# Kernel tuning notes

Measured on AMD Instinct MI355X. Metric: run time of the kernel, lower is better.

The kernel has to match this reference:

```python
import jax, jax.numpy as jnp
import numpy as np

# --- Clifford algebra constants for a 4D Euclidean space (MULTIVECTOR_DIM = 16) ---
# grades 0..4 have dims (1,4,6,4,1); component index -> grade:
GRADE_OF = np.array([0] + [1]*4 + [2]*6 + [3]*4 + [4], dtype=np.int64)  # [16]
# reversion sign per grade k: (-1)^{k(k-1)/2}
_REV_PER_GRADE = np.array([1.0, 1.0, -1.0, -1.0, 1.0], dtype=np.float32)
REVERSION = jnp.asarray(_REV_PER_GRADE[GRADE_OF])            # [16]
# scalar part of geometric product of orthonormal basis blades: diag of reversion signs
SCALAR_TABLE = jnp.asarray(np.diag(_REV_PER_GRADE[GRADE_OF]).astype(np.float32))  # [16,16]
SCALE = 1.0 / np.sqrt(16.0)

B, S, H, M = 4, 2048, 8, 16


def _block_masks():
    block = (GRADE_OF[:, None] == GRADE_OF[None, :]).astype(np.float32)  # [16,16]
    bias = ((GRADE_OF == 0) | (GRADE_OF == 4)).astype(np.float32)        # [16]
    return jnp.asarray(block), jnp.asarray(bias)


def setup_inputs() -> dict:
    key = jax.random.key(0)
    ks = jax.random.split(key, 10)
    block, bias = _block_masks()
    def w_in(k):   # [16, H, 16], zero outside grade blocks (j -> i within same grade)
        return jax.random.normal(k, (M, H, M), jnp.float32) * 0.1 * block[:, None, :]
    def b_in(k):   # [H, 16], only grade-0 / grade-4 components have bias
        return jax.random.normal(k, (H, M), jnp.float32) * 0.1 * bias[None, :]
    x = jax.random.normal(ks[0], (B, S, M), jnp.float32)
    return {
        "x": x,
        "wq": w_in(ks[1]), "bq": b_in(ks[2]),
        "wk": w_in(ks[3]), "bk": b_in(ks[4]),
        "wv": w_in(ks[5]), "bv": b_in(ks[6]),
        "wo": jax.random.normal(ks[7], (H, M, M), jnp.float32) * 0.1 * block[None, :, :],
        "bo": jax.random.normal(ks[8], (M,), jnp.float32) * 0.1 * bias,
    }


def reference(x, wq, bq, wk, bk, wv, bv, wo, bo):
    # per-grade Q/K/V projections, packed as block-sparse linears over 16 components
    q = jnp.einsum('bsj,jhi->bhsi', x, wq) + bq[None, :, None, :]  # [B,H,S,16]
    k = jnp.einsum('bsj,jhi->bhsi', x, wk) + bk[None, :, None, :]
    v = jnp.einsum('bsj,jhi->bhsi', x, wv) + bv[None, :, None, :]
    k_rev = k * REVERSION[None, None, None, :]
    # scalar part of geometric product <Q * reverse(K)>_0 via fixed bilinear table
    scores = jnp.einsum('bhqi,bhkj,ij->bhqk', q, k_rev, SCALAR_TABLE) * SCALE
    attn = jax.nn.softmax(scores, axis=-1)                         # [B,H,S,S]
    head = jnp.einsum('bhqk,bhki->bhqi', attn, v)                  # [B,H,S,16]
    # per-grade output projections (block over heads x grade components)
    out = jnp.einsum('bhqj,hji->bqi', head, wo) + bo               # [B,S,16]
    return out
```

## Files before the change

kernel.cpp:

```cpp
#include <hip/hip_runtime.h>

#define BB 4
#define SS 2048
#define HH 8
#define MM 16

#define QSCALE 0.36067376022224085f

typedef __attribute__((ext_vector_type(8)))  short short8;
typedef __attribute__((ext_vector_type(4)))  int   int4v;
typedef __attribute__((ext_vector_type(4)))  float f32x4;
typedef __attribute__((ext_vector_type(16))) float f32x16;

static constexpr size_t NQKV = (size_t)BB * HH * SS * MM;

__device__ __forceinline__ int pk_bf16(float lo, float hi) {
    int r;
    asm("v_cvt_pk_bf16_f32 %0, %1, %2" : "=v"(r) : "v"(lo), "v"(hi));
    return r;
}

__device__ __forceinline__ void proj16(const float xr[16], const float* __restrict__ w,
                                       const float* __restrict__ bias, int h, float out[16]) {
#pragma unroll
    for (int i = 0; i < 16; i++) out[i] = bias[(h << 4) + i];
#pragma unroll
    for (int j = 0; j < 16; j++) {
        float xj = xr[j];
        const float* wr = w + (((j * HH) + h) << 4);
#pragma unroll
        for (int i = 0; i < 16; i++) out[i] = fmaf(xj, wr[i], out[i]);
    }
}

__device__ __forceinline__ void pack_store(ushort* dst, const float o[16], float scale) {
    int4v w0, w1;
#pragma unroll
    for (int j = 0; j < 4; j++) w0[j] = pk_bf16(o[2*j] * scale,     o[2*j+1] * scale);
#pragma unroll
    for (int j = 0; j < 4; j++) w1[j] = pk_bf16(o[8+2*j] * scale,   o[8+2*j+1] * scale);
    int4v* p = (int4v*)dst;
    p[0] = w0; p[1] = w1;
}

__global__ __launch_bounds__(256) void proj_kernel(
    const float* __restrict__ x,
    const float* __restrict__ wq, const float* __restrict__ bq,
    const float* __restrict__ wk, const float* __restrict__ bk,
    const float* __restrict__ wv, const float* __restrict__ bv,
    ushort* __restrict__ qb, ushort* __restrict__ kb, ushort* __restrict__ vb)
{
    int h  = blockIdx.x >> 5;
    int bs = ((blockIdx.x & 31) << 8) + threadIdx.x;
    int b  = bs >> 11;

    float xr[16];
    const float4* x4 = (const float4*)(x + (size_t)bs * MM);
#pragma unroll
    for (int j = 0; j < 4; j++) {
        float4 t = x4[j];
        xr[j*4+0] = t.x; xr[j*4+1] = t.y; xr[j*4+2] = t.z; xr[j*4+3] = t.w;
    }

    size_t orow = (((size_t)(b * HH + h) * SS) + (bs & 2047)) * MM;
    float o[16];

    proj16(xr, wq, bq, h, o);  pack_store(qb + orow, o, QSCALE);
    proj16(xr, wk, bk, h, o);  pack_store(kb + orow, o, 1.0f);
    proj16(xr, wv, bv, h, o);  pack_store(vb + orow, o, 1.0f);
}

__global__ __launch_bounds__(512) void attn_kernel(
    const ushort* __restrict__ qb, const ushort* __restrict__ kb,
    const ushort* __restrict__ vb, float* __restrict__ hb)
{
    __shared__ ushort stage[4][3840];

    int tid = threadIdx.x;
    int grp = tid >> 7, t7 = tid & 127;
    int wid2 = (tid >> 6) & 1;
    int lane = tid & 63;
    int n = lane & 31, c = lane >> 5;

    int nb = ((blockIdx.x & 7) << 7) | (blockIdx.x >> 3);
    int bh = nb >> 5, qt = nb & 31;
    size_t base = (size_t)bh * SS * MM;
    const ushort* Qg = qb + base;
    const ushort* Kg = kb + base;
    const ushort* Vg = vb + base;

    int q = qt * 64 + wid2 * 32 + n;
    short8 qf = *(const short8*)(Qg + (size_t)q * MM + c * 8);

    ushort* Kl = &stage[grp][0];
    ushort* Vt = &stage[grp][1536];

    for (int i = t7; i < 72; i += 128) {
        Vt[16 * 72 + i] = 0x3F80;
        Vt[20 * 72 + i] = 0x3F80;
#pragma unroll
        for (int r = 17; r < 20; r++) Vt[r * 72 + i] = 0;
#pragma unroll
        for (int r = 21; r < 32; r++) Vt[r * 72 + i] = 0;
    }

    int k0 = grp * 512;
    int srow = t7 >> 1, shalf = t7 & 1;

    {
        int4v kw = *(const int4v*)(Kg + (size_t)(k0 + srow) * MM + shalf * 8);
        int4v vw = *(const int4v*)(Vg + (size_t)(k0 + srow) * MM + shalf * 8);
        *(int4v*)&Kl[srow * 24 + shalf * 8] = kw;
        union { int4v v; ushort s[8]; } vu; vu.v = vw;
#pragma unroll
        for (int j = 0; j < 8; j++) Vt[(8 * shalf + j) * 72 + srow] = vu.s[j];
    }
    __syncthreads();

    f32x16 oacc = 0;
    const f32x16 zacc = 0;
    float cs = 0.0f;
    int csd = lane >> 2, cspart = lane & 3;

    for (int t = 0; t < 8; t++) {
        int4v kw2, vw2;
        if (t != 7) {
            kw2 = *(const int4v*)(Kg + (size_t)(k0 + (t + 1) * 64 + srow) * MM + shalf * 8);
            vw2 = *(const int4v*)(Vg + (size_t)(k0 + (t + 1) * 64 + srow) * MM + shalf * 8);
        }

#pragma unroll
        for (int sub = 0; sub < 2; sub++) {
            short8 kf = *(const short8*)&Kl[(sub * 32 + n) * 24 + c * 8];
            short8 vf1 = *(const short8*)&Vt[n * 72 + sub * 32 + c * 8];
            short8 vf2 = *(const short8*)&Vt[n * 72 + sub * 32 + 16 + c * 8];
            f32x16 s = __builtin_amdgcn_mfma_f32_32x32x16_bf16(kf, qf, zacc, 0, 0, 0);

            float p0 = __builtin_amdgcn_exp2f(s[0])  - 1.0f;
            float p1 = __builtin_amdgcn_exp2f(s[1])  - 1.0f;
            float p2 = __builtin_amdgcn_exp2f(s[2])  - 1.0f;
            float p3 = __builtin_amdgcn_exp2f(s[3])  - 1.0f;
            float p4 = __builtin_amdgcn_exp2f(s[4])  - 1.0f;
            float p5 = __builtin_amdgcn_exp2f(s[5])  - 1.0f;
            float p6 = __builtin_amdgcn_exp2f(s[6])  - 1.0f;
            float p7 = __builtin_amdgcn_exp2f(s[7])  - 1.0f;
            int a0 = pk_bf16(p0, p1), a1 = pk_bf16(p2, p3);
            int a2 = pk_bf16(p4, p5), a3 = pk_bf16(p6, p7);
            int w0 = a0, w2 = a2;
            asm("v_permlane32_swap_b32 %0, %1" : "+v"(w0), "+v"(w2));
            int w1 = a1, w3 = a3;
            asm("v_permlane32_swap_b32 %0, %1" : "+v"(w1), "+v"(w3));
            int4v bi1 = {w0, w1, w2, w3};
            short8 B1 = __builtin_bit_cast(short8, bi1);
            oacc = __builtin_amdgcn_mfma_f32_32x32x16_bf16(vf1, B1, oacc, 0, 0, 0);

            float p8  = __builtin_amdgcn_exp2f(s[8])  - 1.0f;
            float p9  = __builtin_amdgcn_exp2f(s[9])  - 1.0f;
            float p10 = __builtin_amdgcn_exp2f(s[10]) - 1.0f;
            float p11 = __builtin_amdgcn_exp2f(s[11]) - 1.0f;
            float p12 = __builtin_amdgcn_exp2f(s[12]) - 1.0f;
            float p13 = __builtin_amdgcn_exp2f(s[13]) - 1.0f;
            float p14 = __builtin_amdgcn_exp2f(s[14]) - 1.0f;
            float p15 = __builtin_amdgcn_exp2f(s[15]) - 1.0f;
            int a4 = pk_bf16(p8,  p9),  a5 = pk_bf16(p10, p11);
            int a6 = pk_bf16(p12, p13), a7 = pk_bf16(p14, p15);
            int u0 = a4, u2 = a6;
            asm("v_permlane32_swap_b32 %0, %1" : "+v"(u0), "+v"(u2));
            int u1 = a5, u3 = a7;
            asm("v_permlane32_swap_b32 %0, %1" : "+v"(u1), "+v"(u3));
            int4v bi2 = {u0, u1, u2, u3};
            short8 B2 = __builtin_bit_cast(short8, bi2);
            oacc = __builtin_amdgcn_mfma_f32_32x32x16_bf16(vf2, B2, oacc, 0, 0, 0);
        }

        {
            int4v u0 = *(const int4v*)&Vt[csd * 72 + cspart * 16];
            int4v u1 = *(const int4v*)&Vt[csd * 72 + cspart * 16 + 8];
#pragma unroll
            for (int j = 0; j < 4; j++) {
                cs += __builtin_bit_cast(float, u0[j] << 16);
                cs += __builtin_bit_cast(float, (int)(u0[j] & 0xFFFF0000));
                cs += __builtin_bit_cast(float, u1[j] << 16);
                cs += __builtin_bit_cast(float, (int)(u1[j] & 0xFFFF0000));
            }
        }

        __syncthreads();
        if (t != 7) {
            *(int4v*)&Kl[srow * 24 + shalf * 8] = kw2;
            union { int4v v; ushort s[8]; } vu; vu.v = vw2;
#pragma unroll
            for (int j = 0; j < 8; j++) Vt[(8 * shalf + j) * 72 + srow] = vu.s[j];
        }
        __syncthreads();
    }

    cs += __shfl_xor(cs, 1);
    cs += __shfl_xor(cs, 2);

    float* mgf = (float*)&stage[0][0];
    int ql = wid2 * 32 + n;
    if (grp != 0) {
        float* dst = mgf + (size_t)(grp - 1) * 1152 + ql * 18;
#pragma unroll
        for (int j = 0; j < 4; j++) dst[4 * c + j]     = oacc[j];
#pragma unroll
        for (int j = 0; j < 4; j++) dst[8 + 4 * c + j] = oacc[4 + j];
        dst[16 + c] = oacc[8];
    }
    if (wid2 == 0 && cspart == 0) mgf[3456 + grp * 16 + csd] = cs;
    __syncthreads();

    if (grp == 0) {
        float l = oacc[8];
        float o0[4], o1[4];
#pragma unroll
        for (int j = 0; j < 4; j++) { o0[j] = oacc[j]; o1[j] = oacc[4 + j]; }
#pragma unroll
        for (int p = 0; p < 3; p++) {
            const float* src = mgf + (size_t)p * 1152 + ql * 18;
#pragma unroll
            for (int j = 0; j < 4; j++) o0[j] += src[4 * c + j];
#pragma unroll
            for (int j = 0; j < 4; j++) o1[j] += src[8 + 4 * c + j];
            l += src[16 + c];
        }
#pragma unroll
        for (int w = 0; w < 4; w++) {
#pragma unroll
            for (int j = 0; j < 4; j++) o0[j] += mgf[3456 + w * 16 + 4 * c + j];
#pragma unroll
            for (int j = 0; j < 4; j++) o1[j] += mgf[3456 + w * 16 + 8 + 4 * c + j];
        }
        l += 2048.0f;

        float inv = 1.0f / l;
        float* orow = hb + base + (size_t)q * MM;
        f32x4 v0 = {o0[0] * inv, o0[1] * inv, o0[2] * inv, o0[3] * inv};
        f32x4 v1 = {o1[0] * inv, o1[1] * inv, o1[2] * inv, o1[3] * inv};
        *(f32x4*)(orow + 4 * c) = v0;
        *(f32x4*)(orow + 8 + 4 * c) = v1;
    }
}

__global__ __launch_bounds__(128) void outproj_kernel(
    const float* __restrict__ hb, const float* __restrict__ wo,
    const float* __restrict__ bo, float* __restrict__ out)
{
    int tid = threadIdx.x;
    int row = blockIdx.x * 64 + (tid >> 1);
    int hh = tid & 1;
    int b = row >> 11, s = row & 2047;

    float acc[16];
#pragma unroll
    for (int i = 0; i < 16; i++) acc[i] = 0.0f;

    for (int hi = 0; hi < 4; hi++) {
        int h = hh * 4 + hi;
        const float* hr = hb + ((size_t)(b * 8 + h) * SS + s) * MM;
        float hv[16];
        const f32x4* h4 = (const f32x4*)hr;
#pragma unroll
        for (int j = 0; j < 4; j++) {
            f32x4 tv = h4[j];
            hv[j*4+0] = tv[0]; hv[j*4+1] = tv[1]; hv[j*4+2] = tv[2]; hv[j*4+3] = tv[3];
        }
#pragma unroll
        for (int j = 0; j < 16; j++) {
            float hj = hv[j];
            const float* wr = wo + (((h << 4) + j) << 4);
#pragma unroll
            for (int i = 0; i < 16; i++) acc[i] = fmaf(hj, wr[i], acc[i]);
        }
    }

#pragma unroll
    for (int i = 0; i < 16; i++) acc[i] += __shfl_xor(acc[i], 1);

    if (hh == 0) {
        float* op = out + (size_t)row * MM;
#pragma unroll
        for (int j = 0; j < 4; j++) {
            f32x4 v = {acc[4*j+0] + bo[4*j+0], acc[4*j+1] + bo[4*j+1],
                       acc[4*j+2] + bo[4*j+2], acc[4*j+3] + bo[4*j+3]};
            *(f32x4*)(op + 4*j) = v;
        }
    }
}

extern "C" void kernel_launch(void* const* d_in, const int* in_sizes, int n_in,
                              void* d_out, int out_size, void* d_ws, size_t ws_size,
                              hipStream_t stream) {
    const float* x  = (const float*)d_in[0];
    const float* wq = (const float*)d_in[1];
    const float* bq = (const float*)d_in[2];
    const float* wk = (const float*)d_in[3];
    const float* bk = (const float*)d_in[4];
    const float* wv = (const float*)d_in[5];
    const float* bv = (const float*)d_in[6];
    const float* wo = (const float*)d_in[7];
    const float* bo = (const float*)d_in[8];
    float* out = (float*)d_out;

    ushort* qb = (ushort*)d_ws;
    ushort* kb = qb + NQKV;
    ushort* vb = kb + NQKV;
    float*  hb = (float*)(vb + NQKV);

    proj_kernel<<<256, 256, 0, stream>>>(x, wq, bq, wk, bk, wv, bv, qb, kb, vb);
    attn_kernel<<<1024, 512, 0, stream>>>(qb, kb, vb, hb);
    outproj_kernel<<<128, 128, 0, stream>>>(hb, wo, bo, out);
}
```

Baseline: 52.70 us.

## Process two query tiles per wave with double-buffered 128-key K/V stages

Each wave now holds two 32-query fragments and reuses every K/V fragment loaded from LDS for both, halving LDS reads per score. Keys are split across 2 groups instead of 4, with 128-key tiles that are double-buffered, so one barrier per iteration replaces two. Blocks shrink to 256 threads and the grid to 512 blocks, which lowers the number of waves available to hide latency and raises register pressure from the two accumulators.

Result: no change. 52.53 us (-0.3%).

```diff
diff --git a/kernel.cpp b/kernel.cpp
--- a/kernel.cpp
+++ b/kernel.cpp
@@ -70,112 +70,172 @@
     proj16(xr, wv, bv, h, o);  pack_store(vb + orow, o, 1.0f);
 }
 
-__global__ __launch_bounds__(512) void attn_kernel(
+__global__ __launch_bounds__(256) void attn_kernel(
     const ushort* __restrict__ qb, const ushort* __restrict__ kb,
     const ushort* __restrict__ vb, float* __restrict__ hb)
 {
-    __shared__ ushort stage[4][3840];
+    __shared__ ushort stage[2][2][7424];
 
     int tid = threadIdx.x;
-    int grp = tid >> 7, t7 = tid & 127;
-    int wid2 = (tid >> 6) & 1;
+    int w = tid >> 6, grp = w >> 1, qw = w & 1;
     int lane = tid & 63;
     int n = lane & 31, c = lane >> 5;
-
-    int nb = ((blockIdx.x & 7) << 7) | (blockIdx.x >> 3);
-    int bh = nb >> 5, qt = nb & 31;
+    int t7 = tid & 127;
+
+    int nb = ((blockIdx.x & 7) << 6) | (blockIdx.x >> 3);
+    int bh = nb >> 4, qt = nb & 15;
     size_t base = (size_t)bh * SS * MM;
     const ushort* Qg = qb + base;
     const ushort* Kg = kb + base;
     const ushort* Vg = vb + base;
 
-    int q = qt * 64 + wid2 * 32 + n;
-    short8 qf = *(const short8*)(Qg + (size_t)q * MM + c * 8);
-
-    ushort* Kl = &stage[grp][0];
-    ushort* Vt = &stage[grp][1536];
-
-    for (int i = t7; i < 72; i += 128) {
-        Vt[16 * 72 + i] = 0x3F80;
-        Vt[20 * 72 + i] = 0x3F80;
-#pragma unroll
-        for (int r = 17; r < 20; r++) Vt[r * 72 + i] = 0;
-#pragma unroll
-        for (int r = 21; r < 32; r++) Vt[r * 72 + i] = 0;
-    }
-
-    int k0 = grp * 512;
-    int srow = t7 >> 1, shalf = t7 & 1;
+    int qA = qt * 128 + qw * 64 + n;
+    int qB = qA + 32;
+    short8 qfA = *(const short8*)(Qg + (size_t)qA * MM + c * 8);
+    short8 qfB = *(const short8*)(Qg + (size_t)qB * MM + c * 8);
+
+#pragma unroll
+    for (int buf = 0; buf < 2; buf++) {
+        ushort* Vt = &stage[grp][buf][3072];
+        for (int i = t7; i < 136; i += 128) {
+            Vt[16 * 136 + i] = 0x3F80;
+            Vt[20 * 136 + i] = 0x3F80;
+#pragma unroll
+            for (int r = 17; r < 20; r++) Vt[r * 136 + i] = 0;
+#pragma unroll
+            for (int r = 21; r < 32; r++) Vt[r * 136 + i] = 0;
+        }
+    }
+
+    int k0 = grp * 1024;
+    int srow = t7;
 
     {
-        int4v kw = *(const int4v*)(Kg + (size_t)(k0 + srow) * MM + shalf * 8);
-        int4v vw = *(const int4v*)(Vg + (size_t)(k0 + srow) * MM + shalf * 8);
-        *(int4v*)&Kl[srow * 24 + shalf * 8] = kw;
-        union { int4v v; ushort s[8]; } vu; vu.v = vw;
-#pragma unroll
-        for (int j = 0; j < 8; j++) Vt[(8 * shalf + j) * 72 + srow] = vu.s[j];
+        const ushort* kr = Kg + (size_t)(k0 + srow) * MM;
+        const ushort* vr = Vg + (size_t)(k0 + srow) * MM;
+        int4v kw0 = *(const int4v*)(kr);
+        int4v kw1 = *(const int4v*)(kr + 8);
+        int4v vw0 = *(const int4v*)(vr);
+        int4v vw1 = *(const int4v*)(vr + 8);
+        ushort* Kl = &stage[grp][0][0];
+        ushort* Vt = &stage[grp][0][3072];
+        *(int4v*)&Kl[srow * 24]     = kw0;
+        *(int4v*)&Kl[srow * 24 + 8] = kw1;
+        union { int4v v; ushort s[8]; } ua, ub; ua.v = vw0; ub.v = vw1;
+#pragma unroll
+        for (int j = 0; j < 8; j++) Vt[j * 136 + srow]       = ua.s[j];
+#pragma unroll
+        for (int j = 0; j < 8; j++) Vt[(8 + j) * 136 + srow] = ub.s[j];
     }
     __syncthreads();
 
-    f32x16 oacc = 0;
+    f32x16 oaccA = 0, oaccB = 0;
     const f32x16 zacc = 0;
     float cs = 0.0f;
-    int csd = lane >> 2, cspart = lane & 3;
+    int csd = lane >> 2, csp = lane & 3;
 
     for (int t = 0; t < 8; t++) {
-        int4v kw2, vw2;
+        int cur = t & 1;
+        const ushort* Kl = &stage[grp][cur][0];
+        const ushort* Vt = &stage[grp][cur][3072];
+
+        int4v kw0, kw1, vw0, vw1;
         if (t != 7) {
-            kw2 = *(const int4v*)(Kg + (size_t)(k0 + (t + 1) * 64 + srow) * MM + shalf * 8);
-            vw2 = *(const int4v*)(Vg + (size_t)(k0 + (t + 1) * 64 + srow) * MM + shalf * 8);
-        }
-
-#pragma unroll
-        for (int sub = 0; sub < 2; sub++) {
-            short8 kf = *(const short8*)&Kl[(sub * 32 + n) * 24 + c * 8];
-            short8 vf1 = *(const short8*)&Vt[n * 72 + sub * 32 + c * 8];
-            short8 vf2 = *(const short8*)&Vt[n * 72 + sub * 32 + 16 + c * 8];
-            f32x16 s = __builtin_amdgcn_mfma_f32_32x32x16_bf16(kf, qf, zacc, 0, 0, 0);
-
-            float p0 = __builtin_amdgcn_exp2f(s[0])  - 1.0f;
-            float p1 = __builtin_amdgcn_exp2f(s[1])  - 1.0f;
-            float p2 = __builtin_amdgcn_exp2f(s[2])  - 1.0f;
-            float p3 = __builtin_amdgcn_exp2f(s[3])  - 1.0f;
-            float p4 = __builtin_amdgcn_exp2f(s[4])  - 1.0f;
-            float p5 = __builtin_amdgcn_exp2f(s[5])  - 1.0f;
-            float p6 = __builtin_amdgcn_exp2f(s[6])  - 1.0f;
-            float p7 = __builtin_amdgcn_exp2f(s[7])  - 1.0f;
-            int a0 = pk_bf16(p0, p1), a1 = pk_bf16(p2, p3);
-            int a2 = pk_bf16(p4, p5), a3 = pk_bf16(p6, p7);
-            int w0 = a0, w2 = a2;
-            asm("v_permlane32_swap_b32 %0, %1" : "+v"(w0), "+v"(w2));
-            int w1 = a1, w3 = a3;
-            asm("v_permlane32_swap_b32 %0, %1" : "+v"(w1), "+v"(w3));
-            int4v bi1 = {w0, w1, w2, w3};
-            short8 B1 = __builtin_bit_cast(short8, bi1);
-            oacc = __builtin_amdgcn_mfma_f32_32x32x16_bf16(vf1, B1, oacc, 0, 0, 0);
-
-            float p8  = __builtin_amdgcn_exp2f(s[8])  - 1.0f;
-            float p9  = __builtin_amdgcn_exp2f(s[9])  - 1.0f;
-            float p10 = __builtin_amdgcn_exp2f(s[10]) - 1.0f;
-            float p11 = __builtin_amdgcn_exp2f(s[11]) - 1.0f;
-            float p12 = __builtin_amdgcn_exp2f(s[12]) - 1.0f;
-            float p13 = __builtin_amdgcn_exp2f(s[13]) - 1.0f;
-            float p14 = __builtin_amdgcn_exp2f(s[14]) - 1.0f;
-            float p15 = __builtin_amdgcn_exp2f(s[15]) - 1.0f;
-            int a4 = pk_bf16(p8,  p9),  a5 = pk_bf16(p10, p11);
-            int a6 = pk_bf16(p12, p13), a7 = pk_bf16(p14, p15);
-            int u0 = a4, u2 = a6;
-            asm("v_permlane32_swap_b32 %0, %1" : "+v"(u0), "+v"(u2));
-            int u1 = a5, u3 = a7;
-            asm("v_permlane32_swap_b32 %0, %1" : "+v"(u1), "+v"(u3));
-            int4v bi2 = {u0, u1, u2, u3};
-            short8 B2 = __builtin_bit_cast(short8, bi2);
-            oacc = __builtin_amdgcn_mfma_f32_32x32x16_bf16(vf2, B2, oacc, 0, 0, 0);
+            const ushort* kr = Kg + (size_t)(k0 + (t + 1) * 128 + srow) * MM;
+            const ushort* vr = Vg + (size_t)(k0 + (t + 1) * 128 + srow) * MM;
+            kw0 = *(const int4v*)(kr);
+            kw1 = *(const int4v*)(kr + 8);
+            vw0 = *(const int4v*)(vr);
+            vw1 = *(const int4v*)(vr + 8);
+        }
+
+#pragma unroll
+        for (int sub = 0; sub < 4; sub++) {
+            short8 kf  = *(const short8*)&Kl[(sub * 32 + n) * 24 + c * 8];
+            short8 vf1 = *(const short8*)&Vt[n * 136 + sub * 32 + c * 8];
+            short8 vf2 = *(const short8*)&Vt[n * 136 + sub * 32 + 16 + c * 8];
+
+            f32x16 sA = __builtin_amdgcn_mfma_f32_32x32x16_bf16(kf, qfA, zacc, 0, 0, 0);
+            f32x16 sB = __builtin_amdgcn_mfma_f32_32x32x16_bf16(kf, qfB, zacc, 0, 0, 0);
+
+            {
+                float p0 = __builtin_amdgcn_exp2f(sA[0])  - 1.0f;
+                float p1 = __builtin_amdgcn_exp2f(sA[1])  - 1.0f;
+                float p2 = __builtin_amdgcn_exp2f(sA[2])  - 1.0f;
+                float p3 = __builtin_amdgcn_exp2f(sA[3])  - 1.0f;
+                float p4 = __builtin_amdgcn_exp2f(sA[4])  - 1.0f;
+                float p5 = __builtin_amdgcn_exp2f(sA[5])  - 1.0f;
+                float p6 = __builtin_amdgcn_exp2f(sA[6])  - 1.0f;
+                float p7 = __builtin_amdgcn_exp2f(sA[7])  - 1.0f;
+                int a0 = pk_bf16(p0, p1), a1 = pk_bf16(p2, p3);
+                int a2 = pk_bf16(p4, p5), a3 = pk_bf16(p6, p7);
+                int w0 = a0, w2 = a2;
+                asm("v_permlane32_swap_b32 %0, %1" : "+v"(w0), "+v"(w2));
+                int w1 = a1, w3 = a3;
+                asm("v_permlane32_swap_b32 %0, %1" : "+v"(w1), "+v"(w3));
+                int4v bi1 = {w0, w1, w2, w3};
+                oaccA = __builtin_amdgcn_mfma_f32_32x32x16_bf16(
+                    vf1, __builtin_bit_cast(short8, bi1), oaccA, 0, 0, 0);
+                float p8  = __builtin_amdgcn_exp2f(sA[8])  - 1.0f;
+                float p9  = __builtin_amdgcn_exp2f(sA[9])  - 1.0f;
+                float p10 = __builtin_amdgcn_exp2f(sA[10]) - 1.0f;
+                float p11 = __builtin_amdgcn_exp2f(sA[11]) - 1.0f;
+                float p12 = __builtin_amdgcn_exp2f(sA[12]) - 1.0f;
+                float p13 = __builtin_amdgcn_exp2f(sA[13]) - 1.0f;
+                float p14 = __builtin_amdgcn_exp2f(sA[14]) - 1.0f;
+                float p15 = __builtin_amdgcn_exp2f(sA[15]) - 1.0f;
+                int a4 = pk_bf16(p8,  p9),  a5 = pk_bf16(p10, p11);
+                int a6 = pk_bf16(p12, p13), a7 = pk_bf16(p14, p15);
+                int u0 = a4, u2 = a6;
+                asm("v_permlane32_swap_b32 %0, %1" : "+v"(u0), "+v"(u2));
+                int u1 = a5, u3 = a7;
+                asm("v_permlane32_swap_b32 %0, %1" : "+v"(u1), "+v"(u3));
+                int4v bi2 = {u0, u1, u2, u3};
+                oaccA = __builtin_amdgcn_mfma_f32_32x32x16_bf16(
+                    vf2, __builtin_bit_cast(short8, bi2), oaccA, 0, 0, 0);
+            }
+            {
+                float p0 = __builtin_amdgcn_exp2f(sB[0])  - 1.0f;
+                float p1 = __builtin_amdgcn_exp2f(sB[1])  - 1.0f;
+                float p2 = __builtin_amdgcn_exp2f(sB[2])  - 1.0f;
+                float p3 = __builtin_amdgcn_exp2f(sB[3])  - 1.0f;
+                float p4 = __builtin_amdgcn_exp2f(sB[4])  - 1.0f;
+                float p5 = __builtin_amdgcn_exp2f(sB[5])  - 1.0f;
+                float p6 = __builtin_amdgcn_exp2f(sB[6])  - 1.0f;
+                float p7 = __builtin_amdgcn_exp2f(sB[7])  - 1.0f;
+                int a0 = pk_bf16(p0, p1), a1 = pk_bf16(p2, p3);
+                int a2 = pk_bf16(p4, p5), a3 = pk_bf16(p6, p7);
+                int w0 = a0, w2 = a2;
+                asm("v_permlane32_swap_b32 %0, %1" : "+v"(w0), "+v"(w2));
+                int w1 = a1, w3 = a3;
+                asm("v_permlane32_swap_b32 %0, %1" : "+v"(w1), "+v"(w3));
+                int4v bi1 = {w0, w1, w2, w3};
+                oaccB = __builtin_amdgcn_mfma_f32_32x32x16_bf16(
+                    vf1, __builtin_bit_cast(short8, bi1), oaccB, 0, 0, 0);
+                float p8  = __builtin_amdgcn_exp2f(sB[8])  - 1.0f;
+                float p9  = __builtin_amdgcn_exp2f(sB[9])  - 1.0f;
+                float p10 = __builtin_amdgcn_exp2f(sB[10]) - 1.0f;
+                float p11 = __builtin_amdgcn_exp2f(sB[11]) - 1.0f;
+                float p12 = __builtin_amdgcn_exp2f(sB[12]) - 1.0f;
+                float p13 = __builtin_amdgcn_exp2f(sB[13]) - 1.0f;
+                float p14 = __builtin_amdgcn_exp2f(sB[14]) - 1.0f;
+                float p15 = __builtin_amdgcn_exp2f(sB[15]) - 1.0f;
+                int a4 = pk_bf16(p8,  p9),  a5 = pk_bf16(p10, p11);
+                int a6 = pk_bf16(p12, p13), a7 = pk_bf16(p14, p15);
+                int u0 = a4, u2 = a6;
+                asm("v_permlane32_swap_b32 %0, %1" : "+v"(u0), "+v"(u2));
+                int u1 = a5, u3 = a7;
+                asm("v_permlane32_swap_b32 %0, %1" : "+v"(u1), "+v"(u3));
+                int4v bi2 = {u0, u1, u2, u3};
+                oaccB = __builtin_amdgcn_mfma_f32_32x32x16_bf16(
+                    vf2, __builtin_bit_cast(short8, bi2), oaccB, 0, 0, 0);
+            }
         }
 
         {
-            int4v u0 = *(const int4v*)&Vt[csd * 72 + cspart * 16];
-            int4v u1 = *(const int4v*)&Vt[csd * 72 + cspart * 16 + 8];
+            const ushort* vrow = &Vt[csd * 136 + qw * 64 + csp * 16];
+            int4v u0 = *(const int4v*)(vrow);
+            int4v u1 = *(const int4v*)(vrow + 8);
 #pragma unroll
             for (int j = 0; j < 4; j++) {
                 cs += __builtin_bit_cast(float, u0[j] << 16);
@@ -185,12 +245,16 @@
             }
         }
 
-        __syncthreads();
         if (t != 7) {
-            *(int4v*)&Kl[srow * 24 + shalf * 8] = kw2;
-            union { int4v v; ushort s[8]; } vu; vu.v = vw2;
-#pragma unroll
-            for (int j = 0; j < 8; j++) Vt[(8 * shalf + j) * 72 + srow] = vu.s[j];
+            ushort* Kl2 = &stage[grp][cur ^ 1][0];
+            ushort* Vt2 = &stage[grp][cur ^ 1][3072];
+            *(int4v*)&Kl2[srow * 24]     = kw0;
+            *(int4v*)&Kl2[srow * 24 + 8] = kw1;
+            union { int4v v; ushort s[8]; } ua, ub; ua.v = vw0; ub.v = vw1;
+#pragma unroll
+            for (int j = 0; j < 8; j++) Vt2[j * 136 + srow]       = ua.s[j];
+#pragma unroll
+            for (int j = 0; j < 8; j++) Vt2[(8 + j) * 136 + srow] = ub.s[j];
         }
         __syncthreads();
     }
@@ -198,48 +262,71 @@
     cs += __shfl_xor(cs, 1);
     cs += __shfl_xor(cs, 2);
 
-    float* mgf = (float*)&stage[0][0];
-    int ql = wid2 * 32 + n;
-    if (grp != 0) {
-        float* dst = mgf + (size_t)(grp - 1) * 1152 + ql * 18;
-#pragma unroll
-        for (int j = 0; j < 4; j++) dst[4 * c + j]     = oacc[j];
-#pragma unroll
-        for (int j = 0; j < 4; j++) dst[8 + 4 * c + j] = oacc[4 + j];
-        dst[16 + c] = oacc[8];
-    }
-    if (wid2 == 0 && cspart == 0) mgf[3456 + grp * 16 + csd] = cs;
+    float* mgf = (float*)&stage[0][0][0];
+    int qlA = qw * 64 + n, qlB = qlA + 32;
+
+    if (grp == 1) {
+        float* dstA = mgf + qlA * 18;
+#pragma unroll
+        for (int j = 0; j < 4; j++) dstA[4 * c + j]     = oaccA[j];
+#pragma unroll
+        for (int j = 0; j < 4; j++) dstA[8 + 4 * c + j] = oaccA[4 + j];
+        dstA[16 + c] = oaccA[8];
+        float* dstB = mgf + qlB * 18;
+#pragma unroll
+        for (int j = 0; j < 4; j++) dstB[4 * c + j]     = oaccB[j];
+#pragma unroll
+        for (int j = 0; j < 4; j++) dstB[8 + 4 * c + j] = oaccB[4 + j];
+        dstB[16 + c] = oaccB[8];
+    }
+    if (csp == 0) mgf[2304 + (grp * 2 + qw) * 16 + csd] = cs;
     __syncthreads();
 
     if (grp == 0) {
-        float l = oacc[8];
-        float o0[4], o1[4];
-#pragma unroll
-        for (int j = 0; j < 4; j++) { o0[j] = oacc[j]; o1[j] = oacc[4 + j]; }
-#pragma unroll
-        for (int p = 0; p < 3; p++) {
-            const float* src = mgf + (size_t)p * 1152 + ql * 18;
-#pragma unroll
-            for (int j = 0; j < 4; j++) o0[j] += src[4 * c + j];
-#pragma unroll
-            for (int j = 0; j < 4; j++) o1[j] += src[8 + 4 * c + j];
-            l += src[16 + c];
-        }
-#pragma unroll
-        for (int w = 0; w < 4; w++) {
-#pragma unroll
-            for (int j = 0; j < 4; j++) o0[j] += mgf[3456 + w * 16 + 4 * c + j];
-#pragma unroll
-            for (int j = 0; j < 4; j++) o1[j] += mgf[3456 + w * 16 + 8 + 4 * c + j];
-        }
-        l += 2048.0f;
-
-        float inv = 1.0f / l;
-        float* orow = hb + base + (size_t)q * MM;
-        f32x4 v0 = {o0[0] * inv, o0[1] * inv, o0[2] * inv, o0[3] * inv};
-        f32x4 v1 = {o1[0] * inv, o1[1] * inv, o1[2] * inv, o1[3] * inv};
-        *(f32x4*)(orow + 4 * c) = v0;
-        *(f32x4*)(orow + 8 + 4 * c) = v1;
+        {
+            const float* src = mgf + qlA * 18;
+            float l = oaccA[8] + src[16 + c] + 2048.0f;
+            float o0[4], o1[4];
+#pragma unroll
+            for (int j = 0; j < 4; j++) o0[j] = oaccA[j]     + src[4 * c + j];
+#pragma unroll
+            for (int j = 0; j < 4; j++) o1[j] = oaccA[4 + j] + src[8 + 4 * c + j];
+#pragma unroll
+            for (int s = 0; s < 4; s++) {
+#pragma unroll
+                for (int j = 0; j < 4; j++) o0[j] += mgf[2304 + s * 16 + 4 * c + j];
+#pragma unroll
+                for (int j = 0; j < 4; j++) o1[j] += mgf[2304 + s * 16 + 8 + 4 * c + j];
+            }
+            float inv = 1.0f / l;
+            float* orow = hb + base + (size_t)qA * MM;
+            f32x4 v0 = {o0[0] * inv, o0[1] * inv, o0[2] * inv, o0[3] * inv};
+            f32x4 v1 = {o1[0] * inv, o1[1] * inv, o1[2] * inv, o1[3] * inv};
+            *(f32x4*)(orow + 4 * c) = v0;
+            *(f32x4*)(orow + 8 + 4 * c) = v1;
+        }
+        {
+            const float* src = mgf + qlB * 18;
+            float l = oaccB[8] + src[16 + c] + 2048.0f;
+            float o0[4], o1[4];
+#pragma unroll
+            for (int j = 0; j < 4; j++) o0[j] = oaccB[j]     + src[4 * c + j];
+#pragma unroll
+            for (int j = 0; j < 4; j++) o1[j] = oaccB[4 + j] + src[8 + 4 * c + j];
+#pragma unroll
+            for (int s = 0; s < 4; s++) {
+#pragma unroll
+                for (int j = 0; j < 4; j++) o0[j] += mgf[2304 + s * 16 + 4 * c + j];
+#pragma unroll
+                for (int j = 0; j < 4; j++) o1[j] += mgf[2304 + s * 16 + 8 + 4 * c + j];
+            }
+            float inv = 1.0f / l;
+            float* orow = hb + base + (size_t)qB * MM;
+            f32x4 v0 = {o0[0] * inv, o0[1] * inv, o0[2] * inv, o0[3] * inv};
+            f32x4 v1 = {o1[0] * inv, o1[1] * inv, o1[2] * inv, o1[3] * inv};
+            *(f32x4*)(orow + 4 * c) = v0;
+            *(f32x4*)(orow + 8 + 4 * c) = v1;
+        }
     }
 }
 
@@ -309,6 +396,6 @@
     float*  hb = (float*)(vb + NQKV);
 
     proj_kernel<<<256, 256, 0, stream>>>(x, wq, bq, wk, bk, wv, bv, qb, kb, vb);
-    attn_kernel<<<1024, 512, 0, stream>>>(qb, kb, vb, hb);
+    attn_kernel<<<512, 256, 0, stream>>>(qb, kb, vb, hb);
     outproj_kernel<<<128, 128, 0, stream>>>(hb, wo, bo, out);
 }
```

## Double attention K/V tile size, split warps by query half, widen outproj grid

Applied to the files above, without the earlier changes.

The attention kernel now stages 128 keys per tile instead of 64, using a new K layout split into two 8-column halves and a wider transposed V stride. This halves the loop trip count and removes one barrier per iteration. Each query-half warp now computes its own column sums, and a waves-per-EU hint of 6 is added to launch bounds. The output projection splits heads across 4 threads per row with an extra shuffle reduction and twice as many blocks, which raises parallelism. The cost is larger LDS use per block, which could limit occupancy.

Result: slower. 93.69 us (+77.8%).

```diff
diff --git a/kernel.cpp b/kernel.cpp
--- a/kernel.cpp
+++ b/kernel.cpp
@@ -70,17 +70,17 @@
     proj16(xr, wv, bv, h, o);  pack_store(vb + orow, o, 1.0f);
 }
 
-__global__ __launch_bounds__(512) void attn_kernel(
+__global__ __launch_bounds__(512, 6) void attn_kernel(
     const ushort* __restrict__ qb, const ushort* __restrict__ kb,
     const ushort* __restrict__ vb, float* __restrict__ hb)
 {
-    __shared__ ushort stage[4][3840];
+    __shared__ ushort stage[4][6400];
 
     int tid = threadIdx.x;
-    int grp = tid >> 7, t7 = tid & 127;
-    int wid2 = (tid >> 6) & 1;
+    int w = tid >> 6, grp = w >> 1, qw = w & 1;
     int lane = tid & 63;
     int n = lane & 31, c = lane >> 5;
+    int t7 = tid & 127;
 
     int nb = ((blockIdx.x & 7) << 7) | (blockIdx.x >> 3);
     int bh = nb >> 5, qt = nb & 31;
@@ -89,51 +89,63 @@
     const ushort* Kg = kb + base;
     const ushort* Vg = vb + base;
 
-    int q = qt * 64 + wid2 * 32 + n;
+    int q = qt * 64 + qw * 32 + n;
     short8 qf = *(const short8*)(Qg + (size_t)q * MM + c * 8);
 
     ushort* Kl = &stage[grp][0];
-    ushort* Vt = &stage[grp][1536];
-
-    for (int i = t7; i < 72; i += 128) {
-        Vt[16 * 72 + i] = 0x3F80;
-        Vt[20 * 72 + i] = 0x3F80;
-#pragma unroll
-        for (int r = 17; r < 20; r++) Vt[r * 72 + i] = 0;
-#pragma unroll
-        for (int r = 21; r < 32; r++) Vt[r * 72 + i] = 0;
+    ushort* Vt = &stage[grp][2048];
+
+    for (int i = t7; i < 136; i += 128) {
+        Vt[16 * 136 + i] = 0x3F80;
+        Vt[20 * 136 + i] = 0x3F80;
+#pragma unroll
+        for (int r = 17; r < 20; r++) Vt[r * 136 + i] = 0;
+#pragma unroll
+        for (int r = 21; r < 32; r++) Vt[r * 136 + i] = 0;
     }
 
     int k0 = grp * 512;
-    int srow = t7 >> 1, shalf = t7 & 1;
+    int srow = t7;
 
     {
-        int4v kw = *(const int4v*)(Kg + (size_t)(k0 + srow) * MM + shalf * 8);
-        int4v vw = *(const int4v*)(Vg + (size_t)(k0 + srow) * MM + shalf * 8);
-        *(int4v*)&Kl[srow * 24 + shalf * 8] = kw;
-        union { int4v v; ushort s[8]; } vu; vu.v = vw;
-#pragma unroll
-        for (int j = 0; j < 8; j++) Vt[(8 * shalf + j) * 72 + srow] = vu.s[j];
+        const ushort* kr = Kg + (size_t)(k0 + srow) * MM;
+        const ushort* vr = Vg + (size_t)(k0 + srow) * MM;
+        int4v kw0 = *(const int4v*)(kr);
+        int4v kw1 = *(const int4v*)(kr + 8);
+        int4v vw0 = *(const int4v*)(vr);
+        int4v vw1 = *(const int4v*)(vr + 8);
+        *(int4v*)&Kl[srow * 8]        = kw0;
+        *(int4v*)&Kl[1024 + srow * 8] = kw1;
+        union { int4v v; ushort s[8]; } ua, ub; ua.v = vw0; ub.v = vw1;
+#pragma unroll
+        for (int j = 0; j < 8; j++) Vt[j * 136 + srow]       = ua.s[j];
+#pragma unroll
+        for (int j = 0; j < 8; j++) Vt[(8 + j) * 136 + srow] = ub.s[j];
     }
     __syncthreads();
 
     f32x16 oacc = 0;
     const f32x16 zacc = 0;
     float cs = 0.0f;
-    int csd = lane >> 2, cspart = lane & 3;
-
-    for (int t = 0; t < 8; t++) {
-        int4v kw2, vw2;
-        if (t != 7) {
-            kw2 = *(const int4v*)(Kg + (size_t)(k0 + (t + 1) * 64 + srow) * MM + shalf * 8);
-            vw2 = *(const int4v*)(Vg + (size_t)(k0 + (t + 1) * 64 + srow) * MM + shalf * 8);
-        }
-
-#pragma unroll
-        for (int sub = 0; sub < 2; sub++) {
-            short8 kf = *(const short8*)&Kl[(sub * 32 + n) * 24 + c * 8];
-            short8 vf1 = *(const short8*)&Vt[n * 72 + sub * 32 + c * 8];
-            short8 vf2 = *(const short8*)&Vt[n * 72 + sub * 32 + 16 + c * 8];
+    int csd = lane >> 2, csp = lane & 3;
+
+    for (int t = 0; t < 4; t++) {
+        int4v kw0, kw1, vw0, vw1;
+        if (t != 3) {
+            const ushort* kr = Kg + (size_t)(k0 + (t + 1) * 128 + srow) * MM;
+            const ushort* vr = Vg + (size_t)(k0 + (t + 1) * 128 + srow) * MM;
+            kw0 = *(const int4v*)(kr);
+            kw1 = *(const int4v*)(kr + 8);
+            vw0 = *(const int4v*)(vr);
+            vw1 = *(const int4v*)(vr + 8);
+        }
+
+#pragma unroll
+        for (int sub = 0; sub < 4; sub++) {
+            short8 kf  = *(const short8*)&Kl[c * 1024 + (sub * 32 + n) * 8];
+            short8 vf1 = *(const short8*)&Vt[n * 136 + sub * 32 + c * 8];
+            short8 vf2 = *(const short8*)&Vt[n * 136 + sub * 32 + 16 + c * 8];
+
             f32x16 s = __builtin_amdgcn_mfma_f32_32x32x16_bf16(kf, qf, zacc, 0, 0, 0);
 
             float p0 = __builtin_amdgcn_exp2f(s[0])  - 1.0f;
@@ -151,8 +163,8 @@
             int w1 = a1, w3 = a3;
             asm("v_permlane32_swap_b32 %0, %1" : "+v"(w1), "+v"(w3));
             int4v bi1 = {w0, w1, w2, w3};
-            short8 B1 = __builtin_bit_cast(short8, bi1);
-            oacc = __builtin_amdgcn_mfma_f32_32x32x16_bf16(vf1, B1, oacc, 0, 0, 0);
+            oacc = __builtin_amdgcn_mfma_f32_32x32x16_bf16(
+                vf1, __builtin_bit_cast(short8, bi1), oacc, 0, 0, 0);
 
             float p8  = __builtin_amdgcn_exp2f(s[8])  - 1.0f;
             float p9  = __builtin_amdgcn_exp2f(s[9])  - 1.0f;
@@ -169,13 +181,14 @@
             int u1 = a5, u3 = a7;
             asm("v_permlane32_swap_b32 %0, %1" : "+v"(u1), "+v"(u3));
             int4v bi2 = {u0, u1, u2, u3};
-            short8 B2 = __builtin_bit_cast(short8, bi2);
-            oacc = __builtin_amdgcn_mfma_f32_32x32x16_bf16(vf2, B2, oacc, 0, 0, 0);
+            oacc = __builtin_amdgcn_mfma_f32_32x32x16_bf16(
+                vf2, __builtin_bit_cast(short8, bi2), oacc, 0, 0, 0);
         }
 
         {
-            int4v u0 = *(const int4v*)&Vt[csd * 72 + cspart * 16];
-            int4v u1 = *(const int4v*)&Vt[csd * 72 + cspart * 16 + 8];
+            const ushort* vrow = &Vt[csd * 136 + qw * 64 + csp * 16];
+            int4v u0 = *(const int4v*)(vrow);
+            int4v u1 = *(const int4v*)(vrow + 8);
 #pragma unroll
             for (int j = 0; j < 4; j++) {
                 cs += __builtin_bit_cast(float, u0[j] << 16);
@@ -186,20 +199,24 @@
         }
 
         __syncthreads();
-        if (t != 7) {
-            *(int4v*)&Kl[srow * 24 + shalf * 8] = kw2;
-            union { int4v v; ushort s[8]; } vu; vu.v = vw2;
-#pragma unroll
-            for (int j = 0; j < 8; j++) Vt[(8 * shalf + j) * 72 + srow] = vu.s[j];
-        }
-        __syncthreads();
+        if (t != 3) {
+            *(int4v*)&Kl[srow * 8]        = kw0;
+            *(int4v*)&Kl[1024 + srow * 8] = kw1;
+            union { int4v v; ushort s[8]; } ua, ub; ua.v = vw0; ub.v = vw1;
+#pragma unroll
+            for (int j = 0; j < 8; j++) Vt[j * 136 + srow]       = ua.s[j];
+#pragma unroll
+            for (int j = 0; j < 8; j++) Vt[(8 + j) * 136 + srow] = ub.s[j];
+            __syncthreads();
+        }
     }
 
     cs += __shfl_xor(cs, 1);
     cs += __shfl_xor(cs, 2);
 
     float* mgf = (float*)&stage[0][0];
-    int ql = wid2 * 32 + n;
+    int ql = qw * 32 + n;
+
     if (grp != 0) {
         float* dst = mgf + (size_t)(grp - 1) * 1152 + ql * 18;
 #pragma unroll
@@ -208,7 +225,7 @@
         for (int j = 0; j < 4; j++) dst[8 + 4 * c + j] = oacc[4 + j];
         dst[16 + c] = oacc[8];
     }
-    if (wid2 == 0 && cspart == 0) mgf[3456 + grp * 16 + csd] = cs;
+    if (csp == 0) mgf[3456 + (grp * 2 + qw) * 16 + csd] = cs;
     __syncthreads();
 
     if (grp == 0) {
@@ -226,11 +243,11 @@
             l += src[16 + c];
         }
 #pragma unroll
-        for (int w = 0; w < 4; w++) {
-#pragma unroll
-            for (int j = 0; j < 4; j++) o0[j] += mgf[3456 + w * 16 + 4 * c + j];
-#pragma unroll
-            for (int j = 0; j < 4; j++) o1[j] += mgf[3456 + w * 16 + 8 + 4 * c + j];
+        for (int s = 0; s < 8; s++) {
+#pragma unroll
+            for (int j = 0; j < 4; j++) o0[j] += mgf[3456 + s * 16 + 4 * c + j];
+#pragma unroll
+            for (int j = 0; j < 4; j++) o1[j] += mgf[3456 + s * 16 + 8 + 4 * c + j];
         }
         l += 2048.0f;
 
@@ -248,16 +265,17 @@
     const float* __restrict__ bo, float* __restrict__ out)
 {
     int tid = threadIdx.x;
-    int row = blockIdx.x * 64 + (tid >> 1);
-    int hh = tid & 1;
+    int row = blockIdx.x * 32 + (tid >> 2);
+    int hq = tid & 3;
     int b = row >> 11, s = row & 2047;
 
     float acc[16];
 #pragma unroll
     for (int i = 0; i < 16; i++) acc[i] = 0.0f;
 
-    for (int hi = 0; hi < 4; hi++) {
-        int h = hh * 4 + hi;
+#pragma unroll
+    for (int hi = 0; hi < 2; hi++) {
+        int h = hq * 2 + hi;
         const float* hr = hb + ((size_t)(b * 8 + h) * SS + s) * MM;
         float hv[16];
         const f32x4* h4 = (const f32x4*)hr;
@@ -277,8 +295,10 @@
 
 #pragma unroll
     for (int i = 0; i < 16; i++) acc[i] += __shfl_xor(acc[i], 1);
-
-    if (hh == 0) {
+#pragma unroll
+    for (int i = 0; i < 16; i++) acc[i] += __shfl_xor(acc[i], 2);
+
+    if (hq == 0) {
         float* op = out + (size_t)row * MM;
 #pragma unroll
         for (int j = 0; j < 4; j++) {
@@ -310,5 +330,5 @@
 
     proj_kernel<<<256, 256, 0, stream>>>(x, wq, bq, wk, bk, wv, bv, qb, kb, vb);
     attn_kernel<<<1024, 512, 0, stream>>>(qb, kb, vb, hb);
-    outproj_kernel<<<128, 128, 0, stream>>>(hb, wo, bo, out);
-}
+    outproj_kernel<<<256, 128, 0, stream>>>(hb, wo, bo, out);
+}
```

## Retile attention to 128 queries per block with double-buffered swizzled K/V LDS

Applied to the files above, without the earlier changes.

The attention kernel now has each block handle 128 queries with two key-splitting groups of four waves each, instead of 64 queries with four groups. K/V chunks of 128 keys are double-buffered in LDS, which removes one barrier per iteration, and V is stored transposed with an XOR swizzle and K in a split-half layout to reduce bank conflicts. s_setprio is placed around the MFMAs, the cross-group merge is simplified, and the output projection uses 4 threads per row over 256 blocks. The aim is better K/V reuse per LDS load and fewer syncs, at the cost of more LDS and a grid half the size, which may hurt occupancy.

Result: faster. 50.79 us (-3.6%).

```diff
diff --git a/kernel.cpp b/kernel.cpp
--- a/kernel.cpp
+++ b/kernel.cpp
@@ -74,67 +74,76 @@
     const ushort* __restrict__ qb, const ushort* __restrict__ kb,
     const ushort* __restrict__ vb, float* __restrict__ hb)
 {
-    __shared__ ushort stage[4][3840];
+    __shared__ ushort Kl[2][2][2048];
+    __shared__ ushort Vl[2][2][4352];
 
     int tid = threadIdx.x;
-    int grp = tid >> 7, t7 = tid & 127;
-    int wid2 = (tid >> 6) & 1;
+    int grp = tid >> 8, t8 = tid & 255;
+    int qw = (tid >> 6) & 3;
     int lane = tid & 63;
     int n = lane & 31, c = lane >> 5;
 
-    int nb = ((blockIdx.x & 7) << 7) | (blockIdx.x >> 3);
-    int bh = nb >> 5, qt = nb & 31;
+    int nb = ((blockIdx.x & 7) << 6) | (blockIdx.x >> 3);
+    int bh = nb >> 4, qt = nb & 15;
     size_t base = (size_t)bh * SS * MM;
     const ushort* Qg = qb + base;
     const ushort* Kg = kb + base;
     const ushort* Vg = vb + base;
 
-    int q = qt * 64 + wid2 * 32 + n;
+    int q = qt * 128 + qw * 32 + n;
     short8 qf = *(const short8*)(Qg + (size_t)q * MM + c * 8);
 
-    ushort* Kl = &stage[grp][0];
-    ushort* Vt = &stage[grp][1536];
-
-    for (int i = t7; i < 72; i += 128) {
-        Vt[16 * 72 + i] = 0x3F80;
-        Vt[20 * 72 + i] = 0x3F80;
-#pragma unroll
-        for (int r = 17; r < 20; r++) Vt[r * 72 + i] = 0;
-#pragma unroll
-        for (int r = 21; r < 32; r++) Vt[r * 72 + i] = 0;
-    }
-
-    int k0 = grp * 512;
-    int srow = t7 >> 1, shalf = t7 & 1;
+    for (int i = t8; i < 136; i += 256) {
+        Vl[grp][0][16 * 136 + i] = 0x3F80;
+        Vl[grp][0][20 * 136 + i] = 0x3F80;
+        Vl[grp][1][16 * 136 + i] = 0x3F80;
+        Vl[grp][1][20 * 136 + i] = 0x3F80;
+    }
+
+    int k0 = grp * 1024;
+    int srow = t8 >> 1, shalf = t8 & 1;
+    int vswz0 = srow ^ (shalf == 0 ? 0 : 0);
 
     {
         int4v kw = *(const int4v*)(Kg + (size_t)(k0 + srow) * MM + shalf * 8);
         int4v vw = *(const int4v*)(Vg + (size_t)(k0 + srow) * MM + shalf * 8);
-        *(int4v*)&Kl[srow * 24 + shalf * 8] = kw;
+        *(int4v*)&Kl[grp][0][shalf * 1024 + srow * 8] = kw;
         union { int4v v; ushort s[8]; } vu; vu.v = vw;
 #pragma unroll
-        for (int j = 0; j < 8; j++) Vt[(8 * shalf + j) * 72 + srow] = vu.s[j];
+        for (int j = 0; j < 8; j++) {
+            int row = 8 * shalf + j;
+            Vl[grp][0][row * 136 + (srow ^ (((row >> 3) & 3) << 3))] = vu.s[j];
+        }
     }
     __syncthreads();
 
     f32x16 oacc = 0;
     const f32x16 zacc = 0;
     float cs = 0.0f;
-    int csd = lane >> 2, cspart = lane & 3;
+    int csd = lane >> 2, csp = lane & 3;
+    int vsw_n  = ((n >> 3) & 3) << 3;
+    int vsw_cs = ((csd >> 3) & 3) << 3;
 
     for (int t = 0; t < 8; t++) {
-        int4v kw2, vw2;
+        int cur = t & 1;
+        const ushort* Klp = &Kl[grp][cur][0];
+        const ushort* Vt  = &Vl[grp][cur][0];
+
+        int4v kw, vw;
         if (t != 7) {
-            kw2 = *(const int4v*)(Kg + (size_t)(k0 + (t + 1) * 64 + srow) * MM + shalf * 8);
-            vw2 = *(const int4v*)(Vg + (size_t)(k0 + (t + 1) * 64 + srow) * MM + shalf * 8);
-        }
-
-#pragma unroll
-        for (int sub = 0; sub < 2; sub++) {
-            short8 kf = *(const short8*)&Kl[(sub * 32 + n) * 24 + c * 8];
-            short8 vf1 = *(const short8*)&Vt[n * 72 + sub * 32 + c * 8];
-            short8 vf2 = *(const short8*)&Vt[n * 72 + sub * 32 + 16 + c * 8];
+            kw = *(const int4v*)(Kg + (size_t)(k0 + (t + 1) * 128 + srow) * MM + shalf * 8);
+            vw = *(const int4v*)(Vg + (size_t)(k0 + (t + 1) * 128 + srow) * MM + shalf * 8);
+        }
+
+#pragma unroll
+        for (int sub = 0; sub < 4; sub++) {
+            short8 kf  = *(const short8*)&Klp[c * 1024 + (sub * 32 + n) * 8];
+            short8 vf1 = *(const short8*)&Vt[n * 136 + ((sub * 32 + c * 8) ^ vsw_n)];
+            short8 vf2 = *(const short8*)&Vt[n * 136 + ((sub * 32 + 16 + c * 8) ^ vsw_n)];
+
+            __builtin_amdgcn_s_setprio(1);
             f32x16 s = __builtin_amdgcn_mfma_f32_32x32x16_bf16(kf, qf, zacc, 0, 0, 0);
+            __builtin_amdgcn_s_setprio(0);
 
             float p0 = __builtin_amdgcn_exp2f(s[0])  - 1.0f;
             float p1 = __builtin_amdgcn_exp2f(s[1])  - 1.0f;
@@ -151,8 +160,10 @@
             int w1 = a1, w3 = a3;
             asm("v_permlane32_swap_b32 %0, %1" : "+v"(w1), "+v"(w3));
             int4v bi1 = {w0, w1, w2, w3};
-            short8 B1 = __builtin_bit_cast(short8, bi1);
-            oacc = __builtin_amdgcn_mfma_f32_32x32x16_bf16(vf1, B1, oacc, 0, 0, 0);
+            __builtin_amdgcn_s_setprio(1);
+            oacc = __builtin_amdgcn_mfma_f32_32x32x16_bf16(
+                vf1, __builtin_bit_cast(short8, bi1), oacc, 0, 0, 0);
+            __builtin_amdgcn_s_setprio(0);
 
             float p8  = __builtin_amdgcn_exp2f(s[8])  - 1.0f;
             float p9  = __builtin_amdgcn_exp2f(s[9])  - 1.0f;
@@ -169,28 +180,29 @@
             int u1 = a5, u3 = a7;
             asm("v_permlane32_swap_b32 %0, %1" : "+v"(u1), "+v"(u3));
             int4v bi2 = {u0, u1, u2, u3};
-            short8 B2 = __builtin_bit_cast(short8, bi2);
-            oacc = __builtin_amdgcn_mfma_f32_32x32x16_bf16(vf2, B2, oacc, 0, 0, 0);
+            __builtin_amdgcn_s_setprio(1);
+            oacc = __builtin_amdgcn_mfma_f32_32x32x16_bf16(
+                vf2, __builtin_bit_cast(short8, bi2), oacc, 0, 0, 0);
+            __builtin_amdgcn_s_setprio(0);
         }
 
         {
-            int4v u0 = *(const int4v*)&Vt[csd * 72 + cspart * 16];
-            int4v u1 = *(const int4v*)&Vt[csd * 72 + cspart * 16 + 8];
+            int4v u = *(const int4v*)&Vt[csd * 136 + ((qw * 32 + csp * 8) ^ vsw_cs)];
 #pragma unroll
             for (int j = 0; j < 4; j++) {
-                cs += __builtin_bit_cast(float, u0[j] << 16);
-                cs += __builtin_bit_cast(float, (int)(u0[j] & 0xFFFF0000));
-                cs += __builtin_bit_cast(float, u1[j] << 16);
-                cs += __builtin_bit_cast(float, (int)(u1[j] & 0xFFFF0000));
+                cs += __builtin_bit_cast(float, u[j] << 16);
+                cs += __builtin_bit_cast(float, (int)(u[j] & 0xFFFF0000));
             }
         }
 
-        __syncthreads();
         if (t != 7) {
-            *(int4v*)&Kl[srow * 24 + shalf * 8] = kw2;
-            union { int4v v; ushort s[8]; } vu; vu.v = vw2;
-#pragma unroll
-            for (int j = 0; j < 8; j++) Vt[(8 * shalf + j) * 72 + srow] = vu.s[j];
+            *(int4v*)&Kl[grp][cur ^ 1][shalf * 1024 + srow * 8] = kw;
+            union { int4v v; ushort s[8]; } vu; vu.v = vw;
+#pragma unroll
+            for (int j = 0; j < 8; j++) {
+                int row = 8 * shalf + j;
+                Vl[grp][cur ^ 1][row * 136 + (srow ^ (((row >> 3) & 3) << 3))] = vu.s[j];
+            }
         }
         __syncthreads();
     }
@@ -198,41 +210,35 @@
     cs += __shfl_xor(cs, 1);
     cs += __shfl_xor(cs, 2);
 
-    float* mgf = (float*)&stage[0][0];
-    int ql = wid2 * 32 + n;
-    if (grp != 0) {
-        float* dst = mgf + (size_t)(grp - 1) * 1152 + ql * 18;
+    float* mgf = (float*)&Kl[0][0][0];
+    int ql = qw * 32 + n;
+
+    if (grp == 1) {
+        float* dst = mgf + ql * 18;
 #pragma unroll
         for (int j = 0; j < 4; j++) dst[4 * c + j]     = oacc[j];
 #pragma unroll
         for (int j = 0; j < 4; j++) dst[8 + 4 * c + j] = oacc[4 + j];
         dst[16 + c] = oacc[8];
     }
-    if (wid2 == 0 && cspart == 0) mgf[3456 + grp * 16 + csd] = cs;
+    if (csp == 0) mgf[2304 + (grp * 4 + qw) * 16 + csd] = cs;
     __syncthreads();
 
     if (grp == 0) {
-        float l = oacc[8];
+        const float* src = mgf + ql * 18;
+        float l = oacc[8] + src[16 + c] + 2048.0f;
         float o0[4], o1[4];
 #pragma unroll
-        for (int j = 0; j < 4; j++) { o0[j] = oacc[j]; o1[j] = oacc[4 + j]; }
-#pragma unroll
-        for (int p = 0; p < 3; p++) {
-            const float* src = mgf + (size_t)p * 1152 + ql * 18;
-#pragma unroll
-            for (int j = 0; j < 4; j++) o0[j] += src[4 * c + j];
-#pragma unroll
-            for (int j = 0; j < 4; j++) o1[j] += src[8 + 4 * c + j];
-            l += src[16 + c];
-        }
-#pragma unroll
-        for (int w = 0; w < 4; w++) {
-#pragma unroll
-            for (int j = 0; j < 4; j++) o0[j] += mgf[3456 + w * 16 + 4 * c + j];
-#pragma unroll
-            for (int j = 0; j < 4; j++) o1[j] += mgf[3456 + w * 16 + 8 + 4 * c + j];
-        }
-        l += 2048.0f;
+        for (int j = 0; j < 4; j++) o0[j] = oacc[j]     + src[4 * c + j];
+#pragma unroll
+        for (int j = 0; j < 4; j++) o1[j] = oacc[4 + j] + src[8 + 4 * c + j];
+#pragma unroll
+        for (int s2 = 0; s2 < 8; s2++) {
+#pragma unroll
+            for (int j = 0; j < 4; j++) o0[j] += mgf[2304 + s2 * 16 + 4 * c + j];
+#pragma unroll
+            for (int j = 0; j < 4; j++) o1[j] += mgf[2304 + s2 * 16 + 8 + 4 * c + j];
+        }
 
         float inv = 1.0f / l;
         float* orow = hb + base + (size_t)q * MM;
@@ -248,16 +254,17 @@
     const float* __restrict__ bo, float* __restrict__ out)
 {
     int tid = threadIdx.x;
-    int row = blockIdx.x * 64 + (tid >> 1);
-    int hh = tid & 1;
+    int row = blockIdx.x * 32 + (tid >> 2);
+    int hq = tid & 3;
     int b = row >> 11, s = row & 2047;
 
     float acc[16];
 #pragma unroll
     for (int i = 0; i < 16; i++) acc[i] = 0.0f;
 
-    for (int hi = 0; hi < 4; hi++) {
-        int h = hh * 4 + hi;
+#pragma unroll
+    for (int hi = 0; hi < 2; hi++) {
+        int h = hq * 2 + hi;
         const float* hr = hb + ((size_t)(b * 8 + h) * SS + s) * MM;
         float hv[16];
         const f32x4* h4 = (const f32x4*)hr;
@@ -277,8 +284,10 @@
 
 #pragma unroll
     for (int i = 0; i < 16; i++) acc[i] += __shfl_xor(acc[i], 1);
-
-    if (hh == 0) {
+#pragma unroll
+    for (int i = 0; i < 16; i++) acc[i] += __shfl_xor(acc[i], 2);
+
+    if (hq == 0) {
         float* op = out + (size_t)row * MM;
 #pragma unroll
         for (int j = 0; j < 4; j++) {
@@ -309,6 +318,6 @@
     float*  hb = (float*)(vb + NQKV);
 
     proj_kernel<<<256, 256, 0, stream>>>(x, wq, bq, wk, bk, wv, bv, qb, kb, vb);
-    attn_kernel<<<1024, 512, 0, stream>>>(qb, kb, vb, hb);
-    outproj_kernel<<<128, 128, 0, stream>>>(hb, wo, bo, out);
-}
+    attn_kernel<<<512, 512, 0, stream>>>(qb, kb, vb, hb);
+    outproj_kernel<<<256, 128, 0, stream>>>(hb, wo, bo, out);
+}
```
